# Kernel tuning notes

Measured on AMD Instinct MI355X. Metric: run time of the kernel, lower is better.

## Reference

```python
import jax, jax.numpy as jnp
from jax import lax
import numpy as np

NF = 64      # feature channels
G = 8        # mask groups
NBR = 3      # top-k neighbors
PATCH = 7    # correlation patch size (patches[0])
CORK = 3     # correlation / unfold kernel size
PAD_COR = 1  # (CORK-1)//2
PAD_S = 4    # PAD_COR + (PATCH-1)//2
ADD = 6      # 2*PAD_S - CORK + 1
B, H, W = 4, 96, 96


def leaky(x):
    return jnp.where(x >= 0, x, 0.1 * x)


def _conv(x, w, b, pad):
    y = lax.conv_general_dilated(x, w, (1, 1), [(pad[0], pad[0]), (pad[1], pad[1])],
                                 dimension_numbers=('NCHW', 'OIHW', 'NCHW'))
    return y + b[None, :, None, None]


def _normalize(x, eps=1e-12):
    n = jnp.sqrt(jnp.sum(x * x, axis=1, keepdims=True))
    return x / jnp.maximum(n, eps)


def _correlation(f1, f2):
    # spatial-correlation-sampler: kernel=3, patch=7, stride=1, pad=1, dilations=1
    # out[b, ph*7+pw, i, j] = sum_{c,u,v} f1p[b,c,i+u,j+v] * f2p[b,c,i+u+ph-3, j+v+pw-3]
    # (unnormalized; only topk indices are consumed downstream, so any positive
    #  constant scale is irrelevant)
    Bx, C, Hx, Wx = f1.shape
    f1p = jnp.pad(f1, ((0, 0), (0, 0), (PAD_COR, PAD_COR), (PAD_COR, PAD_COR)))
    f2p = jnp.pad(f2, ((0, 0), (0, 0), (PAD_S, PAD_S), (PAD_S, PAD_S)))
    outs = []
    for ph in range(PATCH):
        for pw in range(PATCH):
            s = jnp.sum(f1p * f2p[:, :, ph:ph + Hx + 2, pw:pw + Wx + 2], axis=1)  # [B,H+2,W+2]
            o = sum(s[:, u:u + Hx, v:v + Wx] for u in range(CORK) for v in range(CORK))
            outs.append(o)
    return jnp.stack(outs, axis=1)  # [B, 49, H, W]


def setup_inputs() -> dict:
    key = jax.random.key(0)
    ks = jax.random.split(key, 16)

    def wt(k, shape):
        fan_in = shape[1] * shape[2] * shape[3]
        return jax.random.normal(k, shape, jnp.float32) * (1.0 / np.sqrt(fan_in))

    return {
        'ref_fea_l': jax.random.normal(ks[0], (B, NF, H, W), jnp.float32),
        'w1': wt(ks[1], (NF, NF * 2, 3, 3)), 'b1': jnp.zeros((NF,), jnp.float32),
        'w2': wt(ks[2], (NF, NF, 3, 3)),     'b2': jnp.zeros((NF,), jnp.float32),
        'w3': wt(ks[3], (NF, NF, 7, 1)),     'b3': jnp.zeros((NF,), jnp.float32),
        'w4': wt(ks[4], (NF, NF, 1, 7)),     'b4': jnp.zeros((NF,), jnp.float32),
        'wm': wt(ks[5], (G * CORK ** 2, NF, 3, 3)), 'bm': jnp.zeros((G * CORK ** 2,), jnp.float32),
        'wnn': wt(ks[6], (NF, NF * NBR, 3, 3)), 'bnn': jnp.zeros((NF,), jnp.float32),
        'wf': wt(ks[7], (NF, NF * 2, 3, 3)),    'bf': jnp.zeros((NF,), jnp.float32),
    }


def reference(ref_fea_l, w1, b1, w2, b2, w3, b3, w4, b4, wm, bm, wnn, bnn, wf, bf):
    Bx, C, Hx, Wx = ref_fea_l.shape
    nbr_fea = ref_fea_l  # aliased in the original forward

    # mask branch
    x = jnp.concatenate([nbr_fea, ref_fea_l], axis=1)
    x = leaky(_conv(x, w1, b1, (1, 1)))
    x = leaky(_conv(x, w2, b2, (1, 1)))
    x = leaky(_conv(x, w3, b3, (3, 0)))
    x = leaky(_conv(x, w4, b4, (0, 3)))
    mask = _conv(x, wm, bm, (1, 1)).reshape(Bx, G, 1, CORK ** 2, Hx, Wx)

    # correlation + topk neighbor displacements
    nref = _normalize(ref_fea_l)
    corr = _correlation(nref, nref)                     # [B,49,H,W]
    _, idx = lax.top_k(corr.transpose(0, 2, 3, 1), NBR)  # [B,H,W,NBR]

    # flat indices into the (H+6)x(W+6) unfold grid
    ph = idx // PATCH
    pw = idx % PATCH
    yy = jnp.arange(Hx)[:, None, None]
    xx = jnp.arange(Wx)[None, :, None]
    flat = ((ph + yy) * (Wx + ADD) + (pw + xx)).reshape(Bx, Hx * Wx * NBR)

    # unfold (im2col) of nbr features with pad 4, then gather chosen 3x3 patches
    nbr_pad = jnp.pad(nbr_fea, ((0, 0), (0, 0), (PAD_S, PAD_S), (PAD_S, PAD_S)))
    patches = lax.conv_general_dilated_patches(nbr_pad, (CORK, CORK), (1, 1), 'VALID',
                                               dimension_numbers=('NCHW', 'OIHW', 'NCHW'))
    pl = patches.reshape(Bx, C * CORK ** 2, -1).transpose(0, 2, 1)  # [B, (H+6)(W+6), C*9]
    gath = jnp.take_along_axis(pl, flat[:, :, None], axis=1)        # [B, HW*NBR, C*9]
    gath = gath.reshape(Bx * Hx * Wx, NBR * C, CORK, CORK)

    # conv over gathered patches then modulated mask-weighted reduce
    g = leaky(_conv(gath, wnn, bnn, (1, 1)))                         # [BHW, C, 3, 3]
    g = g.reshape(Bx, Hx, Wx, C, CORK ** 2).transpose(0, 3, 4, 1, 2)
    g = g.reshape(Bx, G, C // G, CORK ** 2, Hx, Wx)
    agg = leaky(jnp.sum(g * mask, axis=3).reshape(Bx, C, Hx, Wx))

    out = leaky(_conv(jnp.concatenate([ref_fea_l, agg], axis=1), wf, bf, (1, 1)))
    return out
```

## Files before the change

### kernel.cpp

```cpp
#include <hip/hip_runtime.h>
#include <hip/hip_bf16.h>

constexpr int BATCH = 4;
constexpr int H = 96, W = 96, HW = H * W;
constexpr int NBR = 3;

using bf16x8 = __attribute__((ext_vector_type(8))) short;
using f32x4 = __attribute__((ext_vector_type(4))) float;

static __device__ __forceinline__ float leakyf(float x) {
    return x >= 0.f ? x : 0.1f * x;
}

static __device__ __forceinline__ short f2bf(float x) {
    __hip_bfloat16 h = __float2bfloat16(x);
    return *reinterpret_cast<short*>(&h);
}

static __device__ __forceinline__ float bf2f(short s) {
    __hip_bfloat16 h = *reinterpret_cast<__hip_bfloat16*>(&s);
    return __bfloat162float(h);
}

__global__ __launch_bounds__(256) void k_pre(const float* __restrict__ ref,
                                             short* __restrict__ reft,
                                             float* __restrict__ nrt) {
    int p = blockIdx.x * 256 + threadIdx.x;
    if (p >= BATCH * HW) return;
    int b = p / HW, ij = p % HW;
    const float* src = ref + b * 64 * HW + ij;
    float v[64];
    float ss = 0.f;
#pragma unroll
    for (int c = 0; c < 64; ++c) {
        v[c] = src[c * HW];
        ss += v[c] * v[c];
    }
    float inv = 1.f / fmaxf(sqrtf(ss), 1e-12f);
    short* rd = reft + (size_t)p * 64;
#pragma unroll
    for (int cc = 0; cc < 8; ++cc) {
        bf16x8 o;
#pragma unroll
        for (int j = 0; j < 8; ++j) o[j] = f2bf(v[cc * 8 + j]);
        *(bf16x8*)(rd + cc * 8) = o;
    }
    float* nd = nrt + (size_t)p * 64;
#pragma unroll
    for (int c = 0; c < 64; ++c) nd[c] = v[c] * inv;
}

static __device__ __forceinline__ void packw(const float* __restrict__ src,
                                             short* __restrict__ dst, int i,
                                             int OC, int ICt, int ICsrc, int KH,
                                             int KW, int NT, int fold) {
    int e = i & 7, l = (i >> 3) & 63;
    int rest = i >> 9;
    int nt = rest % NT;
    rest /= NT;
    int ICK = ICt >> 5;
    int kk = rest % ICK;
    int tap = rest / ICK;
    int ic = kk * 32 + (l >> 4) * 8 + e;
    int oc = nt * 16 + (l & 15);
    int u = tap / KW, v = tap % KW;
    float val = 0.f;
    if (oc < OC) {
        val = src[((oc * ICsrc + ic) * KH + u) * KW + v];
        if (fold) val += src[((oc * ICsrc + 64 + ic) * KH + u) * KW + v];
    }
    dst[i] = f2bf(val);
}

constexpr int E1 = 36864, E2 = 36864, E3 = 28672, E4 = 28672, E5 = 46080,
              E6 = 73728, E7 = 110592;
constexpr int C1 = E1, C2 = C1 + E2, C3 = C2 + E3, C4 = C3 + E4, C5 = C4 + E5,
              C6 = C5 + E6, C7 = C6 + E7, CT = C7 + 8;
__global__ void k_prep_all(const float* __restrict__ w1,
                           const float* __restrict__ w2,
                           const float* __restrict__ w3,
                           const float* __restrict__ w4,
                           const float* __restrict__ wm,
                           const float* __restrict__ wf,
                           const float* __restrict__ wnn,
                           short* __restrict__ P1, short* __restrict__ P2,
                           short* __restrict__ P3, short* __restrict__ P4,
                           short* __restrict__ PM, short* __restrict__ PF,
                           short* __restrict__ B2, short* __restrict__ zpad) {
    int i = blockIdx.x * 256 + threadIdx.x;
    if (i >= CT) return;
    if (i < C1) {
        packw(w1, P1, i, 64, 64, 128, 3, 3, 4, 1);
    } else if (i < C2) {
        packw(w2, P2, i - C1, 64, 64, 64, 3, 3, 4, 0);
    } else if (i < C3) {
        packw(w3, P3, i - C2, 64, 64, 64, 7, 1, 4, 0);
    } else if (i < C4) {
        packw(w4, P4, i - C3, 64, 64, 64, 1, 7, 4, 0);
    } else if (i < C5) {
        packw(wm, PM, i - C4, 72, 64, 64, 3, 3, 5, 0);
    } else if (i < C6) {
        packw(wf, PF, i - C5, 64, 128, 128, 3, 3, 4, 0);
    } else if (i < C7) {
        int j = i - C6;
        int e = j & 7, l = (j >> 3) & 63;
        int t = (j >> 9) % 9;
        int h2 = (j / (512 * 9)) % 2;
        int n = (j / (512 * 9 * 2)) % 3;
        int nt = j / (512 * 9 * 2 * 3);
        int oc = nt * 16 + (l & 15);
        int c = h2 * 32 + (l >> 4) * 8 + e;
        int u = t / 3, v = t % 3;
        B2[j] = f2bf(wnn[((oc * 192 + n * 64 + c) * 3 + u) * 3 + v]);
    } else {
        zpad[i - C7] = 0;
    }
}

__global__ void k_zfill(float* __restrict__ S) {
    int idx = blockIdx.x * 256 + threadIdx.x;
    if (idx >= BATCH * 24 * 98 * 49) return;
    int xp = idx % 49, x0 = xp * 2, x1 = x0 + 1;
    int y = (idx / 49) % 98;
    int dd = (idx / (49 * 98)) % 24;
    int b = idx / (49 * 98 * 24);
    int d = 25 + dd;
    int dy = d / 7, dx = d % 7;
    float* row = S + ((size_t)(b * 49 + d)) * (98 * 98) + y * 98;
    int yy = y + dy - 3;
    if (yy < 0 || yy >= 98) {
        row[x0] = 0.f;
        row[x1] = 0.f;
    } else {
        if (x0 + dx - 3 < 0 || x0 + dx - 3 >= 98) row[x0] = 0.f;
        if (x1 + dx - 3 < 0 || x1 + dx - 3 >= 98) row[x1] = 0.f;
    }
}

constexpr int CORR_NCOL = 104;
constexpr int CORR_BYTES = (2 * 5 * CORR_NCOL + 2 * 2 * CORR_NCOL) * 16;
static __device__ void corr_tile_body(const float* __restrict__ nrt,
                                      float* __restrict__ S, char* pool,
                                      int blk) {
    float4* f2s = (float4*)pool;
    float4* f1s = f2s + 2 * 5 * CORR_NCOL;
    const int b = blk / 49;
    const int y0 = (blk % 49) * 2;
    const int tid = threadIdx.x;
    const int x = tid % 98, yloc = tid / 98;
    const int y = y0 + yloc;
    float acc[25];
#pragma unroll
    for (int d = 0; d < 25; ++d) acc[d] = 0.f;
    for (int c0 = 0; c0 < 64; c0 += 8) {
        for (int e = tid; e < 2 * 5 * CORR_NCOL; e += 256) {
            int sc = e % CORR_NCOL;
            int r = (e / CORR_NCOL) % 5;
            int g = e / (CORR_NCOL * 5);
            int iy = y0 - 4 + r, ix = sc - 4;
            float4 v = make_float4(0.f, 0.f, 0.f, 0.f);
            if (iy >= 0 && iy < H && ix >= 0 && ix < W)
                v = *(const float4*)(nrt + ((size_t)(b * HW) + iy * W + ix) * 64 +
                                     c0 + g * 4);
            f2s[(g * 5 + r) * CORR_NCOL + sc] = v;
        }
        for (int e = tid; e < 2 * 2 * CORR_NCOL; e += 256) {
            int sc = e % CORR_NCOL;
            int r = (e / CORR_NCOL) % 2;
            int g = e / (CORR_NCOL * 2);
            int iy = y0 - 1 + r, ix = sc - 4;
            float4 v = make_float4(0.f, 0.f, 0.f, 0.f);
            if (iy >= 0 && iy < H && ix >= 0 && ix < W)
                v = *(const float4*)(nrt + ((size_t)(b * HW) + iy * W + ix) * 64 +
                                     c0 + g * 4);
            f1s[(g * 2 + r) * CORR_NCOL + sc] = v;
        }
        __syncthreads();
        if (tid < 196) {
#pragma unroll
            for (int g = 0; g < 2; ++g) {
                float4 a = f1s[(g * 2 + yloc) * CORR_NCOL + (x + 3)];
#pragma unroll
                for (int d = 0; d < 25; ++d) {
                    const int dy = d / 7, dx = d % 7;
                    float4 q = f2s[(g * 5 + yloc + dy) * CORR_NCOL + (x + dx)];
                    acc[d] = fmaf(a.x, q.x,
                                  fmaf(a.y, q.y,
                                       fmaf(a.z, q.z, fmaf(a.w, q.w, acc[d]))));
                }
            }
        }
        __syncthreads();
    }
    if (tid < 196) {
#pragma unroll
        for (int d = 0; d < 25; ++d)
            S[((size_t)(b * 49 + d)) * (98 * 98) + y * 98 + x] = acc[d];
#pragma unroll
        for (int d = 0; d < 24; ++d) {
            const int dy = d / 7, dx = d % 7;
            int y2 = y + dy - 3, x2 = x + dx - 3;
            if (y2 >= 0 && y2 < 98 && x2 >= 0 && x2 < 98)
                S[((size_t)(b * 49 + 48 - d)) * (98 * 98) + y2 * 98 + x2] = acc[d];
        }
    }
}

static __device__ void topk_body(const float* __restrict__ S,
                                 int* __restrict__ idx3, int blk) {
    int p = blk * 256 + threadIdx.x;
    if (p >= BATCH * HW) return;
    int b = p / HW, i = (p % HW) / W, j = p % W;
    float v0 = -1e30f, v1 = -1e30f, v2 = -1e30f;
    int d0 = 0, d1 = 0, d2 = 0;
    for (int d = 0; d < 49; ++d) {
        const float* s = S + ((b * 49 + d) * 98 + i) * 98 + j;
        float v = 0.f;
#pragma unroll
        for (int u = 0; u < 3; ++u)
#pragma unroll
            for (int vv = 0; vv < 3; ++vv) v += s[u * 98 + vv];
        if (v > v0) {
            v2 = v1; d2 = d1; v1 = v0; d1 = d0; v0 = v; d0 = d;
        } else if (v > v1) {
            v2 = v1; d2 = d1; v1 = v; d1 = d;
        } else if (v > v2) {
            v2 = v; d2 = d;
        }
    }
    idx3[p * 3 + 0] = d0;
    idx3[p * 3 + 1] = d1;
    idx3[p * 3 + 2] = d2;
}

template <int KH, int KW, int IC, int OC, int OMODE, bool BLDS, int NSPL, int TAIL>
__global__ __launch_bounds__(256) void k_cmfma(
    const short* __restrict__ inA, const short* __restrict__ inB,
    const short* __restrict__ Bp, const float* __restrict__ bias,
    void* __restrict__ outp, const float* __restrict__ taux,
    float* __restrict__ tS, int* __restrict__ tidx, int convblks) {
    constexpr int TI = 8, TJ = 16;
    constexpr int PH = (KH - 1) / 2, PW = (KW - 1) / 2;
    constexpr int LR = TI + KH - 1, LC = TJ + KW - 1;
    constexpr int ICB = IC * 2;
    constexpr int LS = (ICB == 128) ? 7 : 8;
    constexpr int ICK = IC / 32;
    constexpr int NTF = (OC + 15) / 16;
    constexpr int NTb = NTF / NSPL;
    constexpr int TAPS = KH * KW;
    constexpr int NOCT = ICB / 16;
    constexpr int XS_BYTES = LR * LC * ICB;
    constexpr int BS_BYTES = BLDS ? TAPS * ICK * NTb * 1024 : 16;
    constexpr int CONV_BYTES = XS_BYTES + BS_BYTES;
    constexpr int POOL =
        (TAIL == 1 && CORR_BYTES > CONV_BYTES) ? CORR_BYTES : CONV_BYTES;
    __shared__ __align__(16) char pool[POOL];
    if (TAIL != 0 && (int)blockIdx.x >= convblks) {
        int xb = (int)blockIdx.x - convblks;
        if (TAIL == 1)
            corr_tile_body(taux, tS, pool, xb);
        else
            topk_body(taux, tidx, xb);
        return;
    }
    char* Xs = pool;
    short* Bs = (short*)(pool + XS_BYTES);
    const int lid = blockIdx.x;
    const int tj0 = (lid % 6) * TJ, ti0 = ((lid / 6) % 12) * TI;
    const int zz = lid / 72;
    const int b = zz / NSPL;
    const int nt0 = (zz % NSPL) * NTb;
    const int tid = threadIdx.x;
    if (BLDS) {
        for (int u2 = tid; u2 < TAPS * ICK * NTb * 64; u2 += 256) {
            int l2 = u2 & 63;
            int rest = u2 >> 6;
            int nt = rest % NTb;
            int qk = rest / NTb;
            ((bf16x8*)Bs)[u2] = ((const bf16x8*)Bp)[(qk * NTF + nt0 + nt) * 64 + l2];
        }
    }
    for (int u2 = tid; u2 < LR * LC * NOCT; u2 += 256) {
        int oct = u2 % NOCT;
        int hp = u2 / NOCT;
        int hr = hp / LC, hc = hp % LC;
        int gi = ti0 + hr - PH, gj = tj0 + hc - PW;
        bf16x8 v = {};
        if (gi >= 0 && gi < H && gj >= 0 && gj < W) {
            const short* s = (oct < 8) ? inA : inB;
            v = *(const bf16x8*)(s + (size_t)(b * HW + gi * W + gj) * 64 +
                                 (oct & 7) * 8);
        }
        int byte = hp * ICB + oct * 16;
        byte ^= ((byte >> LS) & 7) << 4;
        *(bf16x8*)(Xs + byte) = v;
    }
    __syncthreads();
    const int wave = tid >> 6, l = tid & 63;
    const int r = l & 15, q = l >> 4;
    const int mt0 = wave * 2;
    int p0 = mt0 * 16 + r, p1 = p0 + 16;
    int li0 = p0 >> 4, lj0 = p0 & 15, li1 = p1 >> 4, lj1 = p1 & 15;
    f32x4 acc[2][NTb] = {};
#pragma unroll
    for (int t = 0; t < TAPS; ++t) {
        const int u = t / KW, v = t % KW;
        int hp0 = (li0 + u) * LC + (lj0 + v);
        int hp1 = (li1 + u) * LC + (lj1 + v);
#pragma unroll
        for (int kk = 0; kk < ICK; ++kk) {
            int ab0 = hp0 * ICB + kk * 64 + q * 16;
            ab0 ^= ((ab0 >> LS) & 7) << 4;
            int ab1 = hp1 * ICB + kk * 64 + q * 16;
            ab1 ^= ((ab1 >> LS) & 7) << 4;
            bf16x8 a0 = *(const bf16x8*)(Xs + ab0);
            bf16x8 a1 = *(const bf16x8*)(Xs + ab1);
            const short* bbase =
                BLDS ? (const short*)Bs + (t * ICK + kk) * NTb * 512 + l * 8
                     : Bp + ((t * ICK + kk) * NTF + nt0) * 512 + l * 8;
#pragma unroll
            for (int nt = 0; nt < NTb; ++nt) {
                bf16x8 bv = *(const bf16x8*)(bbase + nt * 512);
                acc[0][nt] =
                    __builtin_amdgcn_mfma_f32_16x16x32_bf16(a0, bv, acc[0][nt], 0, 0, 0);
                acc[1][nt] =
                    __builtin_amdgcn_mfma_f32_16x16x32_bf16(a1, bv, acc[1][nt], 0, 0, 0);
            }
        }
    }
    const int col = l & 15;
#pragma unroll
    for (int mt = 0; mt < 2; ++mt)
#pragma unroll
        for (int nt = 0; nt < NTb; ++nt) {
            int oc = (nt0 + nt) * 16 + col;
            float bs = (oc < OC) ? bias[oc] : 0.f;
#pragma unroll
            for (int j = 0; j < 4; ++j) {
                int p = (mt0 + mt) * 16 + q * 4 + j;
                int gi = ti0 + (p >> 4), gj = tj0 + (p & 15);
                float val = acc[mt][nt][j] + bs;
                if (OMODE == 0) {
                    val = leakyf(val);
                    *((short*)outp + (size_t)(b * HW + gi * W + gj) * 64 + oc) =
                        f2bf(val);
                } else if (OMODE == 1) {
                    if (oc < 72)
                        *((short*)outp + (size_t)(b * HW + gi * W + gj) * 72 + oc) =
                            f2bf(val);
                } else {
                    val = leakyf(val);
                    *((float*)outp + (size_t)(b * 64 + oc) * HW + gi * W + gj) = val;
                }
            }
        }
}

__global__ __launch_bounds__(512, 4) void k_agg_mfma(
    const short* __restrict__ refT, const int* __restrict__ idx3,
    const short* __restrict__ B2, const float* __restrict__ bnn,
    const short* __restrict__ maskT, const short* __restrict__ zpad,
    short* __restrict__ agg) {
    constexpr int PX = 32;
    constexpr int BUFB = 36864;
    __shared__ short A_lds[2 * 2 * 18 * 64 * 8];
    __shared__ short sgi[PX][NBR], sgj[PX][NBR];
    const int bid = blockIdx.x;
    const int swz = (bid & 7) * ((int)gridDim.x >> 3) + (bid >> 3);
    const int p0 = swz * PX;
    const int b = p0 / HW;
    const int i0 = (p0 % HW) / W;
    const int j0 = p0 % W;
    const int tid = threadIdx.x;
    const int wave = tid >> 6;
    const int lane = tid & 63;
    if (tid < PX * NBR) {
        int px = tid / NBR, n = tid % NBR;
        int d = idx3[(p0 + px) * NBR + n];
        sgi[px][n] = (short)(i0 + d / 7 - 4);
        sgj[px][n] = (short)(j0 + px + d % 7 - 4);
    }
    __syncthreads();

    auto STAGE = [&](int n, int buf) {
        for (int r2 = wave; r2 < 36; r2 += 8) {
            int kkl = r2 % 18;
            int ph = r2 / 18;
            int rs = kkl >> 1;
            int oh = kkl & 1;
            int c = lane ^ (((lane >> 4) & 3) | (((buf * 36 + r2) & 1) << 2));
            int oct = oh * 4 + (c >> 4);
            int px = ph * 16 + (c & 15);
            int gi = sgi[px][n] + rs / 3;
            int gj = sgj[px][n] + rs % 3;
            const short* src = (gi >= 0 && gi < H && gj >= 0 && gj < W)
                                   ? refT + (size_t)(b * HW + gi * W + gj) * 64 +
                                         oct * 8
                                   : zpad;
            __builtin_amdgcn_global_load_lds(
                (const __attribute__((address_space(1))) void*)src,
                (__attribute__((address_space(3))) void*)((char*)A_lds +
                                                          buf * BUFB + r2 * 1024),
                16, 0, 0);
        }
    };

    const int w = wave & 3;
    const int half = wave >> 2;
    f32x4 acc[9] = {};
    const short* Bw = B2 + (size_t)w * (3 * 2 * 9 * 512) + lane * 8;

    auto COMPUTE = [&](int n, int buf) {
#pragma unroll
        for (int h2 = 0; h2 < 2; ++h2) {
            const short* bb = Bw + (n * 2 + h2) * 9 * 512;
            bf16x8 bv[9];
#pragma unroll
            for (int t = 0; t < 9; ++t) bv[t] = *(const bf16x8*)(bb + t * 512);
#pragma unroll
            for (int rs = 0; rs < 9; ++rs) {
                int kkl = rs * 2 + h2;
                int ab = buf * BUFB + ((((half * 18 + kkl) << 6) + lane) << 4);
                ab ^= ((ab >> 8) & 7) << 4;
                bf16x8 a = *(const bf16x8*)((char*)A_lds + ab);
#pragma unroll
                for (int t = 0; t < 9; ++t) {
                    const int y = rs / 3 - t / 3 + 1;
                    const int x = rs % 3 - t % 3 + 1;
                    if (y >= 0 && y < 3 && x >= 0 && x < 3)
                        acc[y * 3 + x] = __builtin_amdgcn_mfma_f32_16x16x32_bf16(
                            a, bv[t], acc[y * 3 + x], 0, 0, 0);
                }
            }
        }
    };

    STAGE(0, 0);
    STAGE(1, 1);
    __syncthreads();
    COMPUTE(0, 0);
    __syncthreads();
    STAGE(2, 0);
    COMPUTE(1, 1);
    __syncthreads();
    COMPUTE(2, 0);

    const int oc = w * 16 + (lane & 15);
    const float bn = bnn[oc];
    const int mrow = (lane >> 4) * 4;
#pragma unroll
    for (int j = 0; j < 4; ++j) {
        int px = half * 16 + mrow + j;
        int ij = i0 * W + j0 + px;
        const short* mb = maskT + (size_t)(b * HW + ij) * 72 + (oc >> 3) * 9;
        float sacc = 0.f;
#pragma unroll
        for (int yx = 0; yx < 9; ++yx) {
            float gv = leakyf(acc[yx][j] + bn);
            sacc += gv * bf2f(mb[yx]);
        }
        agg[(size_t)(b * HW + ij) * 64 + oc] = f2bf(leakyf(sacc));
    }
}

extern "C" void kernel_launch(void* const* d_in, const int* in_sizes, int n_in,
                              void* d_out, int out_size, void* d_ws,
                              size_t ws_size, hipStream_t stream) {
    const float* ref = (const float*)d_in[0];
    const float* w1 = (const float*)d_in[1];
    const float* b1 = (const float*)d_in[2];
    const float* w2 = (const float*)d_in[3];
    const float* b2 = (const float*)d_in[4];
    const float* w3 = (const float*)d_in[5];
    const float* b3 = (const float*)d_in[6];
    const float* w4 = (const float*)d_in[7];
    const float* b4 = (const float*)d_in[8];
    const float* wm = (const float*)d_in[9];
    const float* bm = (const float*)d_in[10];
    const float* wnn = (const float*)d_in[11];
    const float* bnn = (const float*)d_in[12];
    const float* wf = (const float*)d_in[13];
    const float* bf = (const float*)d_in[14];

    char* ws = (char*)d_ws;
    constexpr size_t O_NRT = 0;
    constexpr size_t O_S = O_NRT + (size_t)BATCH * HW * 64 * 4;
    constexpr size_t O_REFT = O_S + (size_t)BATCH * 49 * 98 * 98 * 4;
    constexpr size_t O_X1 = O_REFT + (size_t)BATCH * HW * 64 * 2;
    constexpr size_t O_X2 = O_X1 + (size_t)BATCH * HW * 64 * 2;
    constexpr size_t O_MASKT = O_X2 + (size_t)BATCH * HW * 64 * 2;
    constexpr size_t O_IDX = O_MASKT + (size_t)BATCH * HW * 72 * 2;
    constexpr size_t O_P1 = O_IDX + (size_t)BATCH * HW * 3 * 4;
    constexpr size_t O_P2 = O_P1 + (size_t)E1 * 2;
    constexpr size_t O_P3 = O_P2 + (size_t)E2 * 2;
    constexpr size_t O_P4 = O_P3 + (size_t)E3 * 2;
    constexpr size_t O_PM = O_P4 + (size_t)E4 * 2;
    constexpr size_t O_PF = O_PM + (size_t)E5 * 2;
    constexpr size_t O_B2 = O_PF + (size_t)E6 * 2;
    constexpr size_t O_ZP = O_B2 + (size_t)E7 * 2;

    float* NRT = (float*)(ws + O_NRT);
    float* S = (float*)(ws + O_S);
    short* REFT = (short*)(ws + O_REFT);
    short* X1 = (short*)(ws + O_X1);
    short* X2 = (short*)(ws + O_X2);
    short* MASKT = (short*)(ws + O_MASKT);
    int* IDX = (int*)(ws + O_IDX);
    short* P1 = (short*)(ws + O_P1);
    short* P2 = (short*)(ws + O_P2);
    short* P3 = (short*)(ws + O_P3);
    short* P4 = (short*)(ws + O_P4);
    short* PM = (short*)(ws + O_PM);
    short* PF = (short*)(ws + O_PF);
    short* B2 = (short*)(ws + O_B2);
    short* ZPAD = (short*)(ws + O_ZP);

    constexpr int CONVB = 6 * 12 * BATCH * 4;
    constexpr int CORRB = BATCH * 49;
    constexpr int TOPKB = BATCH * HW / 256;
    constexpr int ZFB = (BATCH * 24 * 98 * 49 + 255) / 256;

    k_pre<<<(BATCH * HW + 255) / 256, 256, 0, stream>>>(ref, REFT, NRT);
    k_prep_all<<<(CT + 255) / 256, 256, 0, stream>>>(w1, w2, w3, w4, wm, wf, wnn,
                                                     P1, P2, P3, P4, PM, PF, B2,
                                                     ZPAD);
    k_zfill<<<ZFB, 256, 0, stream>>>(S);

    k_cmfma<3, 3, 64, 64, 0, true, 4, 1><<<CONVB + CORRB, 256, 0, stream>>>(
        REFT, nullptr, P1, b1, X1, NRT, S, nullptr, CONVB);
    k_cmfma<3, 3, 64, 64, 0, true, 4, 2><<<CONVB + TOPKB, 256, 0, stream>>>(
        X1, nullptr, P2, b2, X2, S, nullptr, IDX, CONVB);
    k_cmfma<7, 1, 64, 64, 0, true, 4, 0><<<CONVB, 256, 0, stream>>>(
        X2, nullptr, P3, b3, X1, nullptr, nullptr, nullptr, CONVB);
    k_cmfma<1, 7, 64, 64, 0, true, 4, 0><<<CONVB, 256, 0, stream>>>(
        X1, nullptr, P4, b4, X2, nullptr, nullptr, nullptr, CONVB);
    k_cmfma<3, 3, 64, 72, 1, true, 5, 0><<<6 * 12 * BATCH * 5, 256, 0, stream>>>(
        X2, nullptr, PM, bm, MASKT, nullptr, nullptr, nullptr, 6 * 12 * BATCH * 5);

    k_agg_mfma<<<BATCH * HW / 32, 512, 0, stream>>>(REFT, IDX, B2, bnn, MASKT,
                                                    ZPAD, X1);

    k_cmfma<3, 3, 128, 64, 2, false, 2, 0><<<6 * 12 * BATCH * 2, 256, 0, stream>>>(
        REFT, X1, PF, bf, d_out, nullptr, nullptr, nullptr, 6 * 12 * BATCH * 2);
}
```

Before: 182.7 us.

## Load gathered patches directly into registers instead of staging through LDS

The aggregation kernel no longer uses the double-buffered LDS staging with global_load_lds and barriers. Each wave now gathers its A-fragments straight from global memory into registers for each neighbor, and blocks shrink from 32 pixels and 512 threads to 16 pixels and 256 threads. This removes LDS traffic and synchronisation and raises the block count. In exchange, loads are no longer overlapped with compute through explicit double-buffering, register pressure goes up, and each wave re-reads the same patches from global memory or cache.

After: 210.6 us. +15.3%, slower.

```diff
diff --git a/kernel.cpp b/kernel.cpp
--- a/kernel.cpp
+++ b/kernel.cpp
@@ -356,15 +356,12 @@
         }
 }
 
-__global__ __launch_bounds__(512, 4) void k_agg_mfma(
+__global__ __launch_bounds__(256) void k_agg_mfma(
     const short* __restrict__ refT, const int* __restrict__ idx3,
     const short* __restrict__ B2, const float* __restrict__ bnn,
     const short* __restrict__ maskT, const short* __restrict__ zpad,
     short* __restrict__ agg) {
-    constexpr int PX = 32;
-    constexpr int BUFB = 36864;
-    __shared__ short A_lds[2 * 2 * 18 * 64 * 8];
-    __shared__ short sgi[PX][NBR], sgj[PX][NBR];
+    constexpr int PX = 16;
     const int bid = blockIdx.x;
     const int swz = (bid & 7) * ((int)gridDim.x >> 3) + (bid >> 3);
     const int p0 = swz * PX;
@@ -374,92 +371,67 @@
     const int tid = threadIdx.x;
     const int wave = tid >> 6;
     const int lane = tid & 63;
-    if (tid < PX * NBR) {
-        int px = tid / NBR, n = tid % NBR;
-        int d = idx3[(p0 + px) * NBR + n];
-        sgi[px][n] = (short)(i0 + d / 7 - 4);
-        sgj[px][n] = (short)(j0 + px + d % 7 - 4);
-    }
-    __syncthreads();
-
-    auto STAGE = [&](int n, int buf) {
-        for (int r2 = wave; r2 < 36; r2 += 8) {
-            int kkl = r2 % 18;
-            int ph = r2 / 18;
-            int rs = kkl >> 1;
-            int oh = kkl & 1;
-            int c = lane ^ (((lane >> 4) & 3) | (((buf * 36 + r2) & 1) << 2));
-            int oct = oh * 4 + (c >> 4);
-            int px = ph * 16 + (c & 15);
-            int gi = sgi[px][n] + rs / 3;
-            int gj = sgj[px][n] + rs % 3;
-            const short* src = (gi >= 0 && gi < H && gj >= 0 && gj < W)
-                                   ? refT + (size_t)(b * HW + gi * W + gj) * 64 +
-                                         oct * 8
-                                   : zpad;
-            __builtin_amdgcn_global_load_lds(
-                (const __attribute__((address_space(1))) void*)src,
-                (__attribute__((address_space(3))) void*)((char*)A_lds +
-                                                          buf * BUFB + r2 * 1024),
-                16, 0, 0);
-        }
-    };
-
-    const int w = wave & 3;
-    const int half = wave >> 2;
+    const int pxl = lane & 15;
+    const int q = lane >> 4;
+    int ib[NBR], jb[NBR];
+#pragma unroll
+    for (int n = 0; n < NBR; ++n) {
+        int d = idx3[(p0 + pxl) * NBR + n];
+        ib[n] = i0 + d / 7 - 4;
+        jb[n] = j0 + pxl + d % 7 - 4;
+    }
     f32x4 acc[9] = {};
-    const short* Bw = B2 + (size_t)w * (3 * 2 * 9 * 512) + lane * 8;
-
-    auto COMPUTE = [&](int n, int buf) {
+    const short* Bw = B2 + (size_t)wave * (3 * 2 * 9 * 512) + lane * 8;
+    for (int n = 0; n < NBR; ++n) {
+        const short* abase =
+            refT + ((size_t)(b * HW) + ib[n] * W + jb[n]) * 64 + q * 8;
+        bool ok[9];
+#pragma unroll
+        for (int rs = 0; rs < 9; ++rs) {
+            int gi = ib[n] + rs / 3, gj = jb[n] + rs % 3;
+            ok[rs] = (gi >= 0 && gi < H && gj >= 0 && gj < W);
+        }
 #pragma unroll
         for (int h2 = 0; h2 < 2; ++h2) {
             const short* bb = Bw + (n * 2 + h2) * 9 * 512;
             bf16x8 bv[9];
 #pragma unroll
             for (int t = 0; t < 9; ++t) bv[t] = *(const bf16x8*)(bb + t * 512);
+            bf16x8 a9[9];
 #pragma unroll
             for (int rs = 0; rs < 9; ++rs) {
-                int kkl = rs * 2 + h2;
-                int ab = buf * BUFB + ((((half * 18 + kkl) << 6) + lane) << 4);
-                ab ^= ((ab >> 8) & 7) << 4;
-                bf16x8 a = *(const bf16x8*)((char*)A_lds + ab);
+                const short* src =
+                    ok[rs] ? abase + ((rs / 3) * W + (rs % 3)) * 64 + h2 * 32
+                           : zpad;
+                a9[rs] = *(const bf16x8*)src;
+            }
+#pragma unroll
+            for (int rs = 0; rs < 9; ++rs) {
 #pragma unroll
                 for (int t = 0; t < 9; ++t) {
                     const int y = rs / 3 - t / 3 + 1;
                     const int x = rs % 3 - t % 3 + 1;
                     if (y >= 0 && y < 3 && x >= 0 && x < 3)
                         acc[y * 3 + x] = __builtin_amdgcn_mfma_f32_16x16x32_bf16(
-                            a, bv[t], acc[y * 3 + x], 0, 0, 0);
+                            a9[rs], bv[t], acc[y * 3 + x], 0, 0, 0);
                 }
             }
         }
-    };
-
-    STAGE(0, 0);
-    STAGE(1, 1);
-    __syncthreads();
-    COMPUTE(0, 0);
-    __syncthreads();
-    STAGE(2, 0);
-    COMPUTE(1, 1);
-    __syncthreads();
-    COMPUTE(2, 0);
-
-    const int oc = w * 16 + (lane & 15);
+    }
+    const int oc = wave * 16 + (lane & 15);
     const float bn = bnn[oc];
     const int mrow = (lane >> 4) * 4;
 #pragma unroll
     for (int j = 0; j < 4; ++j) {
-        int px = half * 16 + mrow + j;
-        int ij = i0 * W + j0 + px;
-        const short* mb = maskT + (size_t)(b * HW + ij) * 72 + (oc >> 3) * 9;
+        int pix = p0 + mrow + j;
+        const short* mb = maskT + (size_t)pix * 72 + (oc >> 3) * 9;
         float sacc = 0.f;
 #pragma unroll
         for (int yx = 0; yx < 9; ++yx) {
             float gv = leakyf(acc[yx][j] + bn);
             sacc += gv * bf2f(mb[yx]);
         }
-        agg[(size_t)(b * HW + ij) * 64 + oc] = f2bf(leakyf(sacc));
+        agg[(size_t)pix * 64 + oc] = f2bf(leakyf(sacc));
     }
 }
 
@@ -537,7 +509,7 @@
     k_cmfma<3, 3, 64, 72, 1, true, 5, 0><<<6 * 12 * BATCH * 5, 256, 0, stream>>>(
         X2, nullptr, PM, bm, MASKT, nullptr, nullptr, nullptr, 6 * 12 * BATCH * 5);
 
-    k_agg_mfma<<<BATCH * HW / 32, 512, 0, stream>>>(REFT, IDX, B2, bnn, MASKT,
+    k_agg_mfma<<<BATCH * HW / 16, 256, 0, stream>>>(REFT, IDX, B2, bnn, MASKT,
                                                     ZPAD, X1);
 
     k_cmfma<3, 3, 128, 64, 2, false, 2, 0><<<6 * 12 * BATCH * 2, 256, 0, stream>>>(
```
